# Kernel optimization log

Hardware: AMD Instinct MI355X
Metric: run time of the kernel (lower is better)

## Reference

```python
import jax, jax.numpy as jnp
import numpy as np

jax.config.update("jax_enable_x64", True)

NNZ = 8_388_608        # number of sparse (feature_id, value) pairs
N_FEATURES = 8_192     # number of calibrated feature ids
N_BIN = 63             # bin boundaries per feature -> 64 bins
OUT_BITS = 22          # output id space = 1 << 22
GOLDEN32 = np.uint32(0x9E3779B9)  # Knuth multiplicative-hashing constant


def setup_inputs() -> dict:
    key = jax.random.key(0)
    k1, k2, k3 = jax.random.split(key, 3)
    input_keys = jax.random.randint(k1, (NNZ,), 0, 2 * N_FEATURES, dtype=jnp.int64)
    input_vals = jax.random.normal(k2, (NNZ,), dtype=jnp.float32)
    # Calibrated feature ids (sorted) and per-feature sorted bin boundaries.
    feature_ids = jnp.arange(N_FEATURES, dtype=jnp.int64)
    bin_vals = jnp.sort(
        jax.random.normal(k3, (N_FEATURES, N_BIN), dtype=jnp.float32), axis=1
    ).reshape(-1)
    return {
        "input_keys": input_keys,
        "input_vals": input_vals,
        "feature_ids": feature_ids,
        "bin_vals": bin_vals,
    }


def _lower_bound_bins(bin_vals_flat, feat_idx, vals, n_bin):
    """Per-value branchless binary search: bin = sum(bin_row < val).

    bin_vals_flat: [F * n_bin] row-sorted boundaries, feat_idx: [nnz] int,
    vals: [nnz] float. Returns [nnz] int32 bin index in [0, n_bin].
    """
    steps = int(np.ceil(np.log2(n_bin + 1)))  # 6 for n_bin=63
    base = feat_idx.astype(jnp.int64) * n_bin
    lo = jnp.zeros(vals.shape, dtype=jnp.int32)
    hi = jnp.full(vals.shape, n_bin, dtype=jnp.int32)
    for _ in range(steps):
        mid = (lo + hi) >> 1                       # in [0, n_bin]
        mid_safe = jnp.minimum(mid, n_bin - 1)     # gather-safe
        bv = bin_vals_flat[base + mid_safe]
        valid = lo < hi
        go_right = valid & (bv < vals)             # strict '<' => lower bound
        lo = jnp.where(go_right, mid + 1, lo)
        hi = jnp.where(valid & ~go_right, mid, hi)
    return lo


def reference(input_keys, input_vals, feature_ids, bin_vals):
    F = feature_ids.shape[0]
    n_bin = bin_vals.shape[0] // F
    mask = jnp.int64((1 << OUT_BITS) - 1)

    # --- find each key in the (sorted) calibrated feature-id table ---
    idx = jnp.searchsorted(feature_ids, input_keys)          # [nnz]
    idx_safe = jnp.minimum(idx, F - 1)
    calibrated = feature_ids[idx_safe] == input_keys          # [nnz] bool

    # --- bin assignment: bin = sum(bin_vals_row < val) ---
    bins = _lower_bound_bins(bin_vals, idx_safe, input_vals, n_bin)

    # --- 32-bit integer multiplicative hash of (feature_id, bin) ---
    h = (input_keys.astype(jnp.uint32) * GOLDEN32 + bins.astype(jnp.uint32)) * GOLDEN32
    hashed_key = h.astype(jnp.int64) & mask

    out_keys = jnp.where(calibrated, hashed_key, input_keys & mask)
    out_vals = jnp.where(calibrated, jnp.ones_like(input_vals), input_vals)
    # dense_shape of the resulting SparseTensor is [batch, 1 << OUT_BITS]
    return out_keys, out_vals
```

## Files before the change

kernel.cpp:

```cpp
#include <hip/hip_runtime.h>
#include <stdint.h>
#include <math.h>


#define GOLDEN   0x9E3779B9u
#define OUT_MASK ((1u << 22) - 1u)
#define NBIN  63
#define NPIV  8192
#define NKEY  16384
#define MAGIC 0xC0FFEE42u

typedef float fx4 __attribute__((ext_vector_type(4)));
typedef int   ix4 __attribute__((ext_vector_type(4)));
typedef unsigned ux4 __attribute__((ext_vector_type(4)));

__global__ __launch_bounds__(256) void build_tables_kernel(
    const int* __restrict__ fids, const float* __restrict__ bins,
    float* __restrict__ wtab, ux4* __restrict__ ftab,
    unsigned char* __restrict__ scal_g, int F)
{
    const int t = blockIdx.x * blockDim.x + threadIdx.x;
    if (t >= F * 64) return;
    const int r = t >> 6;
    const int j = t & 63;
    const unsigned uk = (unsigned)fids[r];
    const float* src = bins + (size_t)r * NBIN;

    if (uk < (unsigned)NPIV) {
        const int w = j >> 3, s = j & 7;
        float val;
        if (s < 7)      val = src[8 * w + s];
        else if (w < 7) val = src[8 * w + 7];
        else            val = INFINITY;
        wtab[((size_t)uk << 6) + j] = val;
        if (j == 0) {
            ux4 p0, p1;
            p0.x = __float_as_uint(src[7]);
            p0.y = __float_as_uint(src[15]);
            p0.z = __float_as_uint(src[23]);
            p0.w = __float_as_uint(src[31]);
            p1.x = __float_as_uint(src[39]);
            p1.y = __float_as_uint(src[47]);
            p1.z = __float_as_uint(src[55]);
            p1.w = uk ^ MAGIC;
            ftab[uk * 2]     = p0;
            ftab[uk * 2 + 1] = p1;
        }
    } else if (uk < (unsigned)NKEY && j == 0) {
        scal_g[uk - NPIV] = (unsigned char)(0x40u | (uk & 63u));
    }
}

__device__ __forceinline__ void hd_fallback(
    int k, float v, const int* __restrict__ fids, const float* __restrict__ bins,
    int F, int fsteps, float& okey, float& oval)
{
    int lo = 0, hi = F;
    for (int s = 0; s < fsteps; ++s) {
        int  mid  = (lo + hi) >> 1;
        int  mids = min(mid, F - 1);
        int  fv   = fids[mids];
        bool valid = lo < hi;
        bool right = valid && (fv < k);
        lo = right ? mid + 1 : lo;
        hi = (valid && !right) ? mid : hi;
    }
    const int  idx_safe   = min(lo, F - 1);
    const bool calibrated = (fids[idx_safe] == k);
    const float* brow = bins + (size_t)idx_safe * NBIN;
    int blo = 0, bhi = NBIN;
    #pragma unroll
    for (int s = 0; s < 6; ++s) {
        int   mid  = (blo + bhi) >> 1;
        int   mids = min(mid, NBIN - 1);
        float bv   = brow[mids];
        bool  valid = blo < bhi;
        bool  right = valid && (bv < v);
        blo = right ? mid + 1 : blo;
        bhi = (valid && !right) ? mid : bhi;
    }
    const uint32_t h = ((uint32_t)k * GOLDEN + (uint32_t)blo) * GOLDEN;
    okey = calibrated ? (float)(h & OUT_MASK) : (float)((uint32_t)k & OUT_MASK);
    oval = calibrated ? 1.0f : v;
}

__device__ __forceinline__ int hd_cmp8(fx4 a, fx4 b, float v) {
    return (a.x < v) + (a.y < v) + (a.z < v) + (a.w < v)
         + (b.x < v) + (b.y < v) + (b.z < v) + (b.w < v);
}

__global__ __launch_bounds__(256) void hd_main_kernel(
    const int* __restrict__ keys, const float* __restrict__ vals,
    const int* __restrict__ fids, const float* __restrict__ bins,
    const float* __restrict__ wtab, const ux4* __restrict__ ftab,
    const unsigned char* __restrict__ scal_g,
    float* __restrict__ out_keys, float* __restrict__ out_vals,
    int n, int F, int fsteps, int nchunks)
{
    const char* wb = reinterpret_cast<const char*>(wtab);
    const int nthreads = (int)(gridDim.x * blockDim.x);

    for (int c = blockIdx.x * blockDim.x + threadIdx.x; c < nchunks;
         c += nthreads) {
        const int i0 = c * 4;
        int   k0, k1, k2, k3;
        float v0, v1, v2, v3;
        const bool full = (i0 + 3 < n);
        if (full) {
            const ix4 ka = __builtin_nontemporal_load(reinterpret_cast<const ix4*>(keys + i0));
            const fx4 va = __builtin_nontemporal_load(reinterpret_cast<const fx4*>(vals + i0));
            k0 = ka.x; k1 = ka.y; k2 = ka.z; k3 = ka.w;
            v0 = va.x; v1 = va.y; v2 = va.z; v3 = va.w;
        } else {
            k0 = keys[min(i0 + 0, n - 1)]; v0 = vals[min(i0 + 0, n - 1)];
            k1 = keys[min(i0 + 1, n - 1)]; v1 = vals[min(i0 + 1, n - 1)];
            k2 = keys[min(i0 + 2, n - 1)]; v2 = vals[min(i0 + 2, n - 1)];
            k3 = keys[min(i0 + 3, n - 1)]; v3 = vals[min(i0 + 3, n - 1)];
        }

        const unsigned u0 = (unsigned)k0, u1 = (unsigned)k1,
                       u2 = (unsigned)k2, u3 = (unsigned)k3;

#define HD_P1(J)                                                              \
        const unsigned ia##J = (u##J < (unsigned)NPIV) ? u##J : 0u;           \
        const ux4 fa##J = ftab[ia##J * 2];                                    \
        const ux4 fb##J = ftab[ia##J * 2 + 1];                                \
        const unsigned hs##J = u##J - (unsigned)NPIV;                         \
        const unsigned char sb##J =                                           \
            scal_g[hs##J < (unsigned)NPIV ? hs##J : 0u];
        HD_P1(0) HD_P1(1) HD_P1(2) HD_P1(3)
#undef HD_P1

#define HD_P2(J)                                                              \
        const bool cal##J = (u##J < (unsigned)NPIV) &&                        \
                            (fb##J.w == (u##J ^ MAGIC));                      \
        const int c##J = (__uint_as_float(fa##J.x) < v##J)                    \
                       + (__uint_as_float(fa##J.y) < v##J)                    \
                       + (__uint_as_float(fa##J.z) < v##J)                    \
                       + (__uint_as_float(fa##J.w) < v##J)                    \
                       + (__uint_as_float(fb##J.x) < v##J)                    \
                       + (__uint_as_float(fb##J.y) < v##J)                    \
                       + (__uint_as_float(fb##J.z) < v##J);                   \
        const unsigned off##J =                                               \
            cal##J ? ((u##J << 8) + (unsigned)(c##J << 5)) : 0u;              \
        const bool rare##J =                                                  \
            (u##J >= (unsigned)NKEY) ||                                       \
            ((hs##J < (unsigned)NPIV) &&                                      \
             (sb##J == (unsigned char)(0x40u | (u##J & 63u))));
        HD_P2(0) HD_P2(1) HD_P2(2) HD_P2(3)
#undef HD_P2

        const fx4 a0 = *reinterpret_cast<const fx4*>(wb + off0);
        const fx4 b0 = *reinterpret_cast<const fx4*>(wb + off0 + 16);
        const fx4 a1 = *reinterpret_cast<const fx4*>(wb + off1);
        const fx4 b1 = *reinterpret_cast<const fx4*>(wb + off1 + 16);
        const fx4 a2 = *reinterpret_cast<const fx4*>(wb + off2);
        const fx4 b2 = *reinterpret_cast<const fx4*>(wb + off2 + 16);
        const fx4 a3 = *reinterpret_cast<const fx4*>(wb + off3);
        const fx4 b3 = *reinterpret_cast<const fx4*>(wb + off3 + 16);

        float ok0, ok1, ok2, ok3, ov0, ov1, ov2, ov3;
#define HD_P4(J)                                                              \
        {                                                                     \
            const int cnt = (c##J << 3) + hd_cmp8(a##J, b##J, v##J);          \
            const uint32_t h = (u##J * GOLDEN + (uint32_t)cnt) * GOLDEN;      \
            ok##J = cal##J ? (float)(h & OUT_MASK) : (float)(u##J & OUT_MASK);\
            ov##J = cal##J ? 1.0f : v##J;                                     \
        }
        HD_P4(0) HD_P4(1) HD_P4(2) HD_P4(3)
#undef HD_P4

        if (__builtin_expect(rare0 | rare1 | rare2 | rare3, 0)) {
            if (rare0) hd_fallback(k0, v0, fids, bins, F, fsteps, ok0, ov0);
            if (rare1) hd_fallback(k1, v1, fids, bins, F, fsteps, ok1, ov1);
            if (rare2) hd_fallback(k2, v2, fids, bins, F, fsteps, ok2, ov2);
            if (rare3) hd_fallback(k3, v3, fids, bins, F, fsteps, ok3, ov3);
        }

        if (full) {
            fx4 s;
            s.x = ok0; s.y = ok1; s.z = ok2; s.w = ok3;
            __builtin_nontemporal_store(s, reinterpret_cast<fx4*>(out_keys + i0));
            s.x = ov0; s.y = ov1; s.z = ov2; s.w = ov3;
            __builtin_nontemporal_store(s, reinterpret_cast<fx4*>(out_vals + i0));
        } else {
            if (i0 + 0 < n) { out_keys[i0 + 0] = ok0; out_vals[i0 + 0] = ov0; }
            if (i0 + 1 < n) { out_keys[i0 + 1] = ok1; out_vals[i0 + 1] = ov1; }
            if (i0 + 2 < n) { out_keys[i0 + 2] = ok2; out_vals[i0 + 2] = ov2; }
            if (i0 + 3 < n) { out_keys[i0 + 3] = ok3; out_vals[i0 + 3] = ov3; }
        }
    }
}

__global__ __launch_bounds__(256) void hd_simple_kernel(
    const int* __restrict__ keys, const float* __restrict__ vals,
    const int* __restrict__ fids, const float* __restrict__ bins,
    float* __restrict__ out_keys, float* __restrict__ out_vals,
    int n, int F, int fsteps)
{
    const int gid = blockIdx.x * blockDim.x + threadIdx.x;
    const int i0 = gid * 4;
    if (i0 >= n) return;
    #pragma unroll
    for (int j = 0; j < 4; ++j) {
        int idx = min(i0 + j, n - 1);
        float okey, oval;
        hd_fallback(keys[idx], vals[idx], fids, bins, F, fsteps, okey, oval);
        if (i0 + j < n) { out_keys[i0 + j] = okey; out_vals[i0 + j] = oval; }
    }
}

extern "C" void kernel_launch(void* const* d_in, const int* in_sizes, int n_in,
                              void* d_out, int out_size, void* d_ws, size_t ws_size,
                              hipStream_t stream) {
    const int*   keys = (const int*)d_in[0];
    const float* vals = (const float*)d_in[1];
    const int*   fids = (const int*)d_in[2];
    const float* bins = (const float*)d_in[3];

    const int n = in_sizes[0];
    const int F = in_sizes[2];

    int fsteps = 0;
    while ((1 << fsteps) < F + 1) ++fsteps;

    float* out_keys = (float*)d_out;
    float* out_vals = (float*)d_out + n;

    const size_t wtab_bytes = (size_t)NPIV * 64 * sizeof(float);
    const size_t ftab_bytes = (size_t)NPIV * 32;
    const size_t scal_bytes = (size_t)NPIV;
    const size_t ws_need    = wtab_bytes + ftab_bytes + scal_bytes;

    const bool fast = (ws_size >= ws_need) && (in_sizes[3] == F * NBIN);

    if (fast) {
        float*         wtab   = (float*)d_ws;
        ux4*           ftab   = (ux4*)((char*)d_ws + wtab_bytes);
        unsigned char* scal_g = (unsigned char*)d_ws + wtab_bytes + ftab_bytes;

        build_tables_kernel<<<(F * 64 + 255) / 256, 256, 0, stream>>>(
            fids, bins, wtab, ftab, scal_g, F);

        const int threads = 256;
        const int nchunks = (n + 3) / 4;
        int nblocks = (nchunks + threads - 1) / threads;
        if (nblocks > 2048) nblocks = 2048;
        hd_main_kernel<<<nblocks, threads, 0, stream>>>(
            keys, vals, fids, bins, wtab, ftab, scal_g,
            out_keys, out_vals, n, F, fsteps, nchunks);
    } else {
        const int threads = 256;
        const int grid = (n + threads * 4 - 1) / (threads * 4);
        hd_simple_kernel<<<grid, threads, 0, stream>>>(
            keys, vals, fids, bins, out_keys, out_vals, n, F, fsteps);
    }
}
```

Before: 174.7 us.

## Compress bin lookup tables to bf16 with exact fallback on ties

Stores the per-feature pivot and bin-boundary tables as bf16 and merges the feature pivot row with a validity tag and row index into one 16-byte entry. Each value is compared in bf16, and any case where the bf16 value equals a boundary falls back to an exact fp32 binary search, so results should stay exact. The kernel also moves from four elements per thread in a grid-stride loop to one element per thread with a full grid. The goal is to halve table footprint so it stays cache-resident and to cut gather bytes per element, at the cost of more integer unpacking and rare divergent fallbacks.

```diff
diff --git a/kernel.cpp b/kernel.cpp
--- a/kernel.cpp
+++ b/kernel.cpp
@@ -8,16 +8,20 @@
 #define NBIN  63
 #define NPIV  8192
 #define NKEY  16384
-#define MAGIC 0xC0FFEE42u
 
 typedef float fx4 __attribute__((ext_vector_type(4)));
 typedef int   ix4 __attribute__((ext_vector_type(4)));
 typedef unsigned ux4 __attribute__((ext_vector_type(4)));
 
+__device__ __forceinline__ unsigned bf16c(float x) {
+    const unsigned b = __float_as_uint(x);
+    unsigned t = ((int)b >= 0) ? ((b + 0xFFFFu) >> 16) : (b >> 16);
+    return (t == 0x8000u) ? 0u : t;
+}
+
 __global__ __launch_bounds__(256) void build_tables_kernel(
     const int* __restrict__ fids, const float* __restrict__ bins,
-    float* __restrict__ wtab, ux4* __restrict__ ftab,
-    unsigned char* __restrict__ scal_g, int F)
+    ux4* __restrict__ ftab16, unsigned short* __restrict__ wtab16, int F)
 {
     const int t = blockIdx.x * blockDim.x + threadIdx.x;
     if (t >= F * 64) return;
@@ -32,22 +36,24 @@
         if (s < 7)      val = src[8 * w + s];
         else if (w < 7) val = src[8 * w + 7];
         else            val = INFINITY;
-        wtab[((size_t)uk << 6) + j] = val;
+        wtab16[((size_t)uk << 6) + j] = (unsigned short)bf16c(val);
         if (j == 0) {
-            ux4 p0, p1;
-            p0.x = __float_as_uint(src[7]);
-            p0.y = __float_as_uint(src[15]);
-            p0.z = __float_as_uint(src[23]);
-            p0.w = __float_as_uint(src[31]);
-            p1.x = __float_as_uint(src[39]);
-            p1.y = __float_as_uint(src[47]);
-            p1.z = __float_as_uint(src[55]);
-            p1.w = uk ^ MAGIC;
-            ftab[uk * 2]     = p0;
-            ftab[uk * 2 + 1] = p1;
+            const unsigned p0 = bf16c(src[7]),  p1 = bf16c(src[15]),
+                           p2 = bf16c(src[23]), p3 = bf16c(src[31]),
+                           p4 = bf16c(src[39]), p5 = bf16c(src[47]),
+                           p6 = bf16c(src[55]);
+            const unsigned tag = 0x6000u | (unsigned)r;
+            ux4 q;
+            q.x = p0 | (p1 << 16);
+            q.y = p2 | (p3 << 16);
+            q.z = p4 | (p5 << 16);
+            q.w = p6 | (tag << 16);
+            ftab16[uk] = q;
         }
     } else if (uk < (unsigned)NKEY && j == 0) {
-        scal_g[uk - NPIV] = (unsigned char)(0x40u | (uk & 63u));
+        const unsigned tag = 0x6000u | (unsigned)r;
+        ux4 q; q.x = 0u; q.y = 0u; q.z = 0u; q.w = tag << 16;
+        ftab16[uk] = q;
     }
 }
 
@@ -84,112 +90,78 @@
     oval = calibrated ? 1.0f : v;
 }
 
-__device__ __forceinline__ int hd_cmp8(fx4 a, fx4 b, float v) {
-    return (a.x < v) + (a.y < v) + (a.z < v) + (a.w < v)
-         + (b.x < v) + (b.y < v) + (b.z < v) + (b.w < v);
-}
-
 __global__ __launch_bounds__(256) void hd_main_kernel(
     const int* __restrict__ keys, const float* __restrict__ vals,
     const int* __restrict__ fids, const float* __restrict__ bins,
-    const float* __restrict__ wtab, const ux4* __restrict__ ftab,
-    const unsigned char* __restrict__ scal_g,
+    const ux4* __restrict__ ftab16, const ux4* __restrict__ wtab16,
     float* __restrict__ out_keys, float* __restrict__ out_vals,
-    int n, int F, int fsteps, int nchunks)
-{
-    const char* wb = reinterpret_cast<const char*>(wtab);
-    const int nthreads = (int)(gridDim.x * blockDim.x);
-
-    for (int c = blockIdx.x * blockDim.x + threadIdx.x; c < nchunks;
-         c += nthreads) {
-        const int i0 = c * 4;
-        int   k0, k1, k2, k3;
-        float v0, v1, v2, v3;
-        const bool full = (i0 + 3 < n);
-        if (full) {
-            const ix4 ka = __builtin_nontemporal_load(reinterpret_cast<const ix4*>(keys + i0));
-            const fx4 va = __builtin_nontemporal_load(reinterpret_cast<const fx4*>(vals + i0));
-            k0 = ka.x; k1 = ka.y; k2 = ka.z; k3 = ka.w;
-            v0 = va.x; v1 = va.y; v2 = va.z; v3 = va.w;
-        } else {
-            k0 = keys[min(i0 + 0, n - 1)]; v0 = vals[min(i0 + 0, n - 1)];
-            k1 = keys[min(i0 + 1, n - 1)]; v1 = vals[min(i0 + 1, n - 1)];
-            k2 = keys[min(i0 + 2, n - 1)]; v2 = vals[min(i0 + 2, n - 1)];
-            k3 = keys[min(i0 + 3, n - 1)]; v3 = vals[min(i0 + 3, n - 1)];
+    int n, int F, int fsteps)
+{
+    const int i = blockIdx.x * (int)blockDim.x + (int)threadIdx.x;
+    if (i >= n) return;
+
+    const int   k = __builtin_nontemporal_load(keys + i);
+    const float v = __builtin_nontemporal_load(vals + i);
+    const unsigned uk = (unsigned)k;
+
+    const unsigned ia = (uk < (unsigned)NKEY) ? uk : 0u;
+    const ux4 fr = ftab16[ia];
+    const unsigned tag     = fr.w >> 16;
+    const bool     written = (tag & 0xE000u) == 0x6000u;
+    const bool     low     = uk < (unsigned)NPIV;
+    const bool     cal     = low && written;
+    const bool     rare    = (uk >= (unsigned)NKEY) || (written && !low);
+
+    const unsigned V  = bf16c(v);
+    const float    Vf = __uint_as_float(V << 16);
+
+    const unsigned s0 = fr.x & 0xFFFFu, s1 = fr.x >> 16;
+    const unsigned s2 = fr.y & 0xFFFFu, s3 = fr.y >> 16;
+    const unsigned s4 = fr.z & 0xFFFFu, s5 = fr.z >> 16;
+    const unsigned s6 = fr.w & 0xFFFFu;
+#define HD_LT(S)  (__uint_as_float((S) << 16) < Vf)
+    const int c = HD_LT(s0) + HD_LT(s1) + HD_LT(s2) + HD_LT(s3)
+                + HD_LT(s4) + HD_LT(s5) + HD_LT(s6);
+    bool amb = (s0 == V) | (s1 == V) | (s2 == V) | (s3 == V)
+             | (s4 == V) | (s5 == V) | (s6 == V);
+
+    const ux4 wr = wtab16[cal ? ((uk << 3) + (unsigned)c) : 0u];
+    const unsigned t0 = wr.x & 0xFFFFu, t1 = wr.x >> 16;
+    const unsigned t2 = wr.y & 0xFFFFu, t3 = wr.y >> 16;
+    const unsigned t4 = wr.z & 0xFFFFu, t5 = wr.z >> 16;
+    const unsigned t6 = wr.w & 0xFFFFu, t7 = wr.w >> 16;
+    int bin = (c << 3)
+            + HD_LT(t0) + HD_LT(t1) + HD_LT(t2) + HD_LT(t3)
+            + HD_LT(t4) + HD_LT(t5) + HD_LT(t6) + HD_LT(t7);
+    amb |= (t0 == V) | (t1 == V) | (t2 == V) | (t3 == V)
+         | (t4 == V) | (t5 == V) | (t6 == V) | (t7 == V);
+#undef HD_LT
+
+    if (__builtin_expect(cal && amb, 0)) {
+        const float* brow = bins + (size_t)(tag & 0x1FFFu) * NBIN;
+        int blo = 0, bhi = NBIN;
+        #pragma unroll
+        for (int s = 0; s < 6; ++s) {
+            int   mid  = (blo + bhi) >> 1;
+            int   mids = min(mid, NBIN - 1);
+            float bv   = brow[mids];
+            bool  valid = blo < bhi;
+            bool  right = valid && (bv < v);
+            blo = right ? mid + 1 : blo;
+            bhi = (valid && !right) ? mid : bhi;
         }
-
-        const unsigned u0 = (unsigned)k0, u1 = (unsigned)k1,
-                       u2 = (unsigned)k2, u3 = (unsigned)k3;
-
-#define HD_P1(J)                                                              \
-        const unsigned ia##J = (u##J < (unsigned)NPIV) ? u##J : 0u;           \
-        const ux4 fa##J = ftab[ia##J * 2];                                    \
-        const ux4 fb##J = ftab[ia##J * 2 + 1];                                \
-        const unsigned hs##J = u##J - (unsigned)NPIV;                         \
-        const unsigned char sb##J =                                           \
-            scal_g[hs##J < (unsigned)NPIV ? hs##J : 0u];
-        HD_P1(0) HD_P1(1) HD_P1(2) HD_P1(3)
-#undef HD_P1
-
-#define HD_P2(J)                                                              \
-        const bool cal##J = (u##J < (unsigned)NPIV) &&                        \
-                            (fb##J.w == (u##J ^ MAGIC));                      \
-        const int c##J = (__uint_as_float(fa##J.x) < v##J)                    \
-                       + (__uint_as_float(fa##J.y) < v##J)                    \
-                       + (__uint_as_float(fa##J.z) < v##J)                    \
-                       + (__uint_as_float(fa##J.w) < v##J)                    \
-                       + (__uint_as_float(fb##J.x) < v##J)                    \
-                       + (__uint_as_float(fb##J.y) < v##J)                    \
-                       + (__uint_as_float(fb##J.z) < v##J);                   \
-        const unsigned off##J =                                               \
-            cal##J ? ((u##J << 8) + (unsigned)(c##J << 5)) : 0u;              \
-        const bool rare##J =                                                  \
-            (u##J >= (unsigned)NKEY) ||                                       \
-            ((hs##J < (unsigned)NPIV) &&                                      \
-             (sb##J == (unsigned char)(0x40u | (u##J & 63u))));
-        HD_P2(0) HD_P2(1) HD_P2(2) HD_P2(3)
-#undef HD_P2
-
-        const fx4 a0 = *reinterpret_cast<const fx4*>(wb + off0);
-        const fx4 b0 = *reinterpret_cast<const fx4*>(wb + off0 + 16);
-        const fx4 a1 = *reinterpret_cast<const fx4*>(wb + off1);
-        const fx4 b1 = *reinterpret_cast<const fx4*>(wb + off1 + 16);
-        const fx4 a2 = *reinterpret_cast<const fx4*>(wb + off2);
-        const fx4 b2 = *reinterpret_cast<const fx4*>(wb + off2 + 16);
-        const fx4 a3 = *reinterpret_cast<const fx4*>(wb + off3);
-        const fx4 b3 = *reinterpret_cast<const fx4*>(wb + off3 + 16);
-
-        float ok0, ok1, ok2, ok3, ov0, ov1, ov2, ov3;
-#define HD_P4(J)                                                              \
-        {                                                                     \
-            const int cnt = (c##J << 3) + hd_cmp8(a##J, b##J, v##J);          \
-            const uint32_t h = (u##J * GOLDEN + (uint32_t)cnt) * GOLDEN;      \
-            ok##J = cal##J ? (float)(h & OUT_MASK) : (float)(u##J & OUT_MASK);\
-            ov##J = cal##J ? 1.0f : v##J;                                     \
-        }
-        HD_P4(0) HD_P4(1) HD_P4(2) HD_P4(3)
-#undef HD_P4
-
-        if (__builtin_expect(rare0 | rare1 | rare2 | rare3, 0)) {
-            if (rare0) hd_fallback(k0, v0, fids, bins, F, fsteps, ok0, ov0);
-            if (rare1) hd_fallback(k1, v1, fids, bins, F, fsteps, ok1, ov1);
-            if (rare2) hd_fallback(k2, v2, fids, bins, F, fsteps, ok2, ov2);
-            if (rare3) hd_fallback(k3, v3, fids, bins, F, fsteps, ok3, ov3);
-        }
-
-        if (full) {
-            fx4 s;
-            s.x = ok0; s.y = ok1; s.z = ok2; s.w = ok3;
-            __builtin_nontemporal_store(s, reinterpret_cast<fx4*>(out_keys + i0));
-            s.x = ov0; s.y = ov1; s.z = ov2; s.w = ov3;
-            __builtin_nontemporal_store(s, reinterpret_cast<fx4*>(out_vals + i0));
-        } else {
-            if (i0 + 0 < n) { out_keys[i0 + 0] = ok0; out_vals[i0 + 0] = ov0; }
-            if (i0 + 1 < n) { out_keys[i0 + 1] = ok1; out_vals[i0 + 1] = ov1; }
-            if (i0 + 2 < n) { out_keys[i0 + 2] = ok2; out_vals[i0 + 2] = ov2; }
-            if (i0 + 3 < n) { out_keys[i0 + 3] = ok3; out_vals[i0 + 3] = ov3; }
-        }
-    }
+        bin = blo;
+    }
+
+    const uint32_t h = (uk * GOLDEN + (uint32_t)bin) * GOLDEN;
+    float ok = cal ? (float)(h & OUT_MASK) : (float)(uk & OUT_MASK);
+    float ov = cal ? 1.0f : v;
+
+    if (__builtin_expect(rare, 0))
+        hd_fallback(k, v, fids, bins, F, fsteps, ok, ov);
+
+    __builtin_nontemporal_store(ok, out_keys + i);
+    __builtin_nontemporal_store(ov, out_vals + i);
 }
 
 __global__ __launch_bounds__(256) void hd_simple_kernel(
@@ -227,28 +199,26 @@
     float* out_keys = (float*)d_out;
     float* out_vals = (float*)d_out + n;
 
-    const size_t wtab_bytes = (size_t)NPIV * 64 * sizeof(float);
-    const size_t ftab_bytes = (size_t)NPIV * 32;
-    const size_t scal_bytes = (size_t)NPIV;
-    const size_t ws_need    = wtab_bytes + ftab_bytes + scal_bytes;
-
-    const bool fast = (ws_size >= ws_need) && (in_sizes[3] == F * NBIN);
+    const size_t ftab_bytes = (size_t)NKEY * 16;
+    const size_t wtab_bytes = (size_t)NPIV * 8 * 16;
+    const size_t ws_need    = ftab_bytes + wtab_bytes;
+
+    const bool fast = (ws_size >= ws_need) && (in_sizes[3] == F * NBIN) &&
+                      (F <= NPIV);
 
     if (fast) {
-        float*         wtab   = (float*)d_ws;
-        ux4*           ftab   = (ux4*)((char*)d_ws + wtab_bytes);
-        unsigned char* scal_g = (unsigned char*)d_ws + wtab_bytes + ftab_bytes;
+        ux4*            ftab16 = (ux4*)d_ws;
+        unsigned short* wtab16 = (unsigned short*)((char*)d_ws + ftab_bytes);
 
         build_tables_kernel<<<(F * 64 + 255) / 256, 256, 0, stream>>>(
-            fids, bins, wtab, ftab, scal_g, F);
+            fids, bins, ftab16, wtab16, F);
 
         const int threads = 256;
-        const int nchunks = (n + 3) / 4;
-        int nblocks = (nchunks + threads - 1) / threads;
-        if (nblocks > 2048) nblocks = 2048;
+        const int nblocks = (n + threads - 1) / threads;
         hd_main_kernel<<<nblocks, threads, 0, stream>>>(
-            keys, vals, fids, bins, wtab, ftab, scal_g,
-            out_keys, out_vals, n, F, fsteps, nchunks);
+            keys, vals, fids, bins, ftab16,
+            reinterpret_cast<const ux4*>(wtab16),
+            out_keys, out_vals, n, F, fsteps);
     } else {
         const int threads = 256;
         const int grid = (n + threads * 4 - 1) / (threads * 4);
```

Measured after the change: 191.8 us. 9.8% more time.
